# Performance work log

Measured on AMD Instinct MI355X. Metric: run time of the kernel, lower is better.

The kernel has to match this reference:

```python
import jax, jax.numpy as jnp
import numpy as np

IN_F = 512
OUT_F = 512

def setup_inputs() -> dict:
    key = jax.random.key(0)
    k1, k2, k3 = jax.random.split(key, 3)
    x = jax.random.normal(k1, (2, 512, IN_F), dtype=jnp.float32)
    # uniform init: a = sqrt(6 / (2 + out_features))
    a = float(np.sqrt(6.0 / (2.0 + OUT_F)))
    W = jax.random.uniform(k2, (OUT_F, IN_F), dtype=jnp.float32, minval=-a, maxval=a)
    bound = float(1.0 / np.sqrt(IN_F))
    b = jax.random.uniform(k3, (OUT_F,), dtype=jnp.float32, minval=-bound, maxval=bound)
    return {"x": x, "W": W, "b": b}

def reference(x, W, b):
    # MAM fully connected (beta == 0 path): for each (row, out-neuron),
    # C = max_k(x_k * w_ok) + min_k(x_k * w_ok), then add bias.
    xf = x.reshape(-1, x.shape[-1])            # (B, in)
    prod = xf[:, None, :] * W[None, :, :]      # (B, out, in) -- the large intermediate
    C = prod.max(axis=-1) + prod.min(axis=-1)  # (B, out)
    C = C + b[None, :]
    return C.reshape(x.shape[:-1] + (W.shape[0],))
```

## Files before the change

### kernel.cpp

```cpp
#include <hip/hip_runtime.h>
#include <math.h>


#define O_TOTAL 512
#define K_TOTAL 512
#define OBLK 64
#define NWAVE 4
#define RPW 2
#define RPB (NWAVE * RPW)
#define KCH 64
#define NCHUNK (K_TOTAL / KCH)

__device__ __forceinline__ void stage16(const float* g, float* lds, int lane) {
#if __has_builtin(__builtin_amdgcn_global_load_lds)
  (void)lane;
  __builtin_amdgcn_global_load_lds(
      (__attribute__((address_space(1))) unsigned int*)g,
      (__attribute__((address_space(3))) unsigned int*)lds, 16, 0, 0);
#else
  *reinterpret_cast<float4*>(lds + lane * 4) = *reinterpret_cast<const float4*>(g);
#endif
}

__global__ __launch_bounds__(256, 4)
void mam_fc_kernel(const float* __restrict__ x, const float* __restrict__ W,
                   const float* __restrict__ bias, float* __restrict__ out) {
  __shared__ float Wl[2][OBLK * KCH];
  __shared__ float Xl[2][RPB * KCH];

  const int t = threadIdx.x;
  const int lane = t & 63;
  const int wv = __builtin_amdgcn_readfirstlane(t >> 6);
  const int ob = blockIdx.x & 7;
  const int rg = blockIdx.x >> 3;
  const int o0 = ob * OBLK;
  const int rowBase = rg * RPB;

  const float* srcW[4];
  int dstWoff[4];
#pragma unroll
  for (int p = 0; p < 4; ++p) {
    const int orow = wv * 16 + p * 4 + (lane >> 4);
    const int g = (lane & 15) ^ (orow & 15);
    srcW[p] = W + (size_t)(o0 + orow) * K_TOTAL + g * 4;
    dstWoff[p] = (wv * 16 + p * 4) * KCH;
  }
  const float* srcX = x + (size_t)(rowBase + wv * 4 + (lane >> 4)) * K_TOTAL + (lane & 15) * 4;
  const int dstXoff = wv * 4 * KCH;

  float amax[RPW][2], amin[RPW][2];
#pragma unroll
  for (int r = 0; r < RPW; ++r) {
#pragma unroll
    for (int p = 0; p < 2; ++p) { amax[r][p] = -INFINITY; amin[r][p] = INFINITY; }
  }

  const unsigned baseW = (unsigned)(lane * (KCH * 4) + (lane & 15) * 16);
  const unsigned baseX = (unsigned)((wv * RPW) * (KCH * 4));

#pragma unroll
  for (int p = 0; p < 4; ++p) stage16(srcW[p], &Wl[0][dstWoff[p]], lane);
  if (wv < 2) stage16(srcX, &Xl[0][dstXoff], lane);
  __syncthreads();

#pragma unroll 1
  for (int c = 0; c < NCHUNK; ++c) {
    if (c + 1 < NCHUNK) {
      const int b = (c + 1) & 1;
      const int kOff = (c + 1) * KCH;
#pragma unroll
      for (int p = 0; p < 4; ++p) stage16(srcW[p] + kOff, &Wl[b][dstWoff[p]], lane);
      if (wv < 2) stage16(srcX + kOff, &Xl[b][dstXoff], lane);
    }

    const char* wb = (const char*)&Wl[c & 1][0];
    const char* xb = (const char*)&Xl[c & 1][0];
#pragma unroll
    for (int j = 0; j < KCH / 4; ++j) {
      const float4 w4 = *reinterpret_cast<const float4*>(wb + (baseW ^ (unsigned)(j * 16)));
#pragma unroll
      for (int r = 0; r < RPW; ++r) {
        const float4 x4 = *reinterpret_cast<const float4*>(xb + baseX + r * (KCH * 4) + j * 16);
        const float p0 = x4.x * w4.x;
        const float p1 = x4.y * w4.y;
        const float p2 = x4.z * w4.z;
        const float p3 = x4.w * w4.w;
        const int par = j & 1;
        amax[r][par] = fmaxf(fmaxf(fmaxf(fmaxf(amax[r][par], p0), p1), p2), p3);
        amin[r][par] = fminf(fminf(fminf(fminf(amin[r][par], p0), p1), p2), p3);
      }
    }
    __syncthreads();
  }

  const float bv = bias[o0 + lane];
#pragma unroll
  for (int r = 0; r < RPW; ++r) {
    const float mm = fmaxf(amax[r][0], amax[r][1]);
    const float nn = fminf(amin[r][0], amin[r][1]);
    out[(size_t)(rowBase + wv * RPW + r) * O_TOTAL + o0 + lane] = mm + nn + bv;
  }
}

extern "C" void kernel_launch(void* const* d_in, const int* in_sizes, int n_in,
                              void* d_out, int out_size, void* d_ws, size_t ws_size,
                              hipStream_t stream) {
  const float* x = (const float*)d_in[0];
  const float* W = (const float*)d_in[1];
  const float* b = (const float*)d_in[2];
  float* out = (float*)d_out;

  const int nrows = in_sizes[0] / K_TOTAL;
  const int nblocks = (O_TOTAL / OBLK) * (nrows / RPB);
  mam_fc_kernel<<<dim3(nblocks), dim3(256), 0, stream>>>(x, W, b, out);
}
```

Before: 22.08 us.

## Swap operand roles: lanes own rows, waves read uniform W rows directly

The kernel is restructured so each lane handles one input row (staged in LDS with an XOR swizzle) and each wave handles four output neurons whose weights are read straight from global memory at wave-uniform addresses, which can become scalar or broadcast loads. Tiles become 64 rows by 16 outputs, giving 512 blocks, and results go through an LDS transpose before a coalesced store with bias. The aim is to cut LDS traffic for W and raise per-lane reuse. The cost is global-load latency for W inside the inner loop, extra LDS for the output transpose, and occupancy hinted lower.

```diff
diff --git a/kernel.cpp b/kernel.cpp
--- a/kernel.cpp
+++ b/kernel.cpp
@@ -4,101 +4,100 @@
 
 #define O_TOTAL 512
 #define K_TOTAL 512
-#define OBLK 64
+#define ROWT 64
 #define NWAVE 4
-#define RPW 2
-#define RPB (NWAVE * RPW)
+#define OPW 4
+#define OUTT (NWAVE * OPW)
 #define KCH 64
 #define NCHUNK (K_TOTAL / KCH)
+#define NJ (KCH / 4)
 
-__device__ __forceinline__ void stage16(const float* g, float* lds, int lane) {
+__device__ __forceinline__ void stage16(const float* g, float* lds_base, int lane) {
 #if __has_builtin(__builtin_amdgcn_global_load_lds)
   (void)lane;
   __builtin_amdgcn_global_load_lds(
       (__attribute__((address_space(1))) unsigned int*)g,
-      (__attribute__((address_space(3))) unsigned int*)lds, 16, 0, 0);
+      (__attribute__((address_space(3))) unsigned int*)lds_base, 16, 0, 0);
 #else
-  *reinterpret_cast<float4*>(lds + lane * 4) = *reinterpret_cast<const float4*>(g);
+  *reinterpret_cast<float4*>(lds_base + lane * 4) = *reinterpret_cast<const float4*>(g);
 #endif
 }
 
-__global__ __launch_bounds__(256, 4)
+__global__ __launch_bounds__(256, 2)
 void mam_fc_kernel(const float* __restrict__ x, const float* __restrict__ W,
                    const float* __restrict__ bias, float* __restrict__ out) {
-  __shared__ float Wl[2][OBLK * KCH];
-  __shared__ float Xl[2][RPB * KCH];
+  __shared__ __align__(16) float Xl[2][ROWT * KCH];
+  __shared__ float Ot[ROWT][OUTT + 1];
 
   const int t = threadIdx.x;
   const int lane = t & 63;
   const int wv = __builtin_amdgcn_readfirstlane(t >> 6);
-  const int ob = blockIdx.x & 7;
-  const int rg = blockIdx.x >> 3;
-  const int o0 = ob * OBLK;
-  const int rowBase = rg * RPB;
+  const int ob = blockIdx.x & 31;
+  const int rg = blockIdx.x >> 5;
+  const int o0 = ob * OUTT;
+  const int row0 = rg * ROWT;
 
-  const float* srcW[4];
-  int dstWoff[4];
+  const float* srcX[4];
 #pragma unroll
   for (int p = 0; p < 4; ++p) {
-    const int orow = wv * 16 + p * 4 + (lane >> 4);
-    const int g = (lane & 15) ^ (orow & 15);
-    srcW[p] = W + (size_t)(o0 + orow) * K_TOTAL + g * 4;
-    dstWoff[p] = (wv * 16 + p * 4) * KCH;
-  }
-  const float* srcX = x + (size_t)(rowBase + wv * 4 + (lane >> 4)) * K_TOTAL + (lane & 15) * 4;
-  const int dstXoff = wv * 4 * KCH;
-
-  float amax[RPW][2], amin[RPW][2];
-#pragma unroll
-  for (int r = 0; r < RPW; ++r) {
-#pragma unroll
-    for (int p = 0; p < 2; ++p) { amax[r][p] = -INFINITY; amin[r][p] = INFINITY; }
+    const int r = wv * 16 + p * 4 + (lane >> 4);
+    const int g = (lane & 15) ^ (r & 15);
+    srcX[p] = x + (size_t)(row0 + r) * K_TOTAL + g * 4;
   }
 
-  const unsigned baseW = (unsigned)(lane * (KCH * 4) + (lane & 15) * 16);
-  const unsigned baseX = (unsigned)((wv * RPW) * (KCH * 4));
+  const float* Wo[OPW];
+#pragma unroll
+  for (int oi = 0; oi < OPW; ++oi)
+    Wo[oi] = W + (size_t)(o0 + wv * OPW + oi) * K_TOTAL;
+
+  float amax[OPW], amin[OPW];
+#pragma unroll
+  for (int oi = 0; oi < OPW; ++oi) { amax[oi] = -INFINITY; amin[oi] = INFINITY; }
+
+  const unsigned baseX = (unsigned)(lane * (KCH * 4) + (lane & 15) * 16);
 
 #pragma unroll
-  for (int p = 0; p < 4; ++p) stage16(srcW[p], &Wl[0][dstWoff[p]], lane);
-  if (wv < 2) stage16(srcX, &Xl[0][dstXoff], lane);
+  for (int p = 0; p < 4; ++p)
+    stage16(srcX[p], &Xl[0][wv * 1024 + p * 256], lane);
   __syncthreads();
 
 #pragma unroll 1
   for (int c = 0; c < NCHUNK; ++c) {
     if (c + 1 < NCHUNK) {
-      const int b = (c + 1) & 1;
       const int kOff = (c + 1) * KCH;
 #pragma unroll
-      for (int p = 0; p < 4; ++p) stage16(srcW[p] + kOff, &Wl[b][dstWoff[p]], lane);
-      if (wv < 2) stage16(srcX + kOff, &Xl[b][dstXoff], lane);
+      for (int p = 0; p < 4; ++p)
+        stage16(srcX[p] + kOff, &Xl[(c + 1) & 1][wv * 1024 + p * 256], lane);
     }
 
-    const char* wb = (const char*)&Wl[c & 1][0];
     const char* xb = (const char*)&Xl[c & 1][0];
 #pragma unroll
-    for (int j = 0; j < KCH / 4; ++j) {
-      const float4 w4 = *reinterpret_cast<const float4*>(wb + (baseW ^ (unsigned)(j * 16)));
+    for (int j = 0; j < NJ; ++j) {
+      const float4 x4 = *reinterpret_cast<const float4*>(xb + (baseX ^ (unsigned)(j * 16)));
 #pragma unroll
-      for (int r = 0; r < RPW; ++r) {
-        const float4 x4 = *reinterpret_cast<const float4*>(xb + baseX + r * (KCH * 4) + j * 16);
+      for (int oi = 0; oi < OPW; ++oi) {
+        const float4 w4 = *reinterpret_cast<const float4*>(Wo[oi] + c * KCH + j * 4);
         const float p0 = x4.x * w4.x;
         const float p1 = x4.y * w4.y;
         const float p2 = x4.z * w4.z;
         const float p3 = x4.w * w4.w;
-        const int par = j & 1;
-        amax[r][par] = fmaxf(fmaxf(fmaxf(fmaxf(amax[r][par], p0), p1), p2), p3);
-        amin[r][par] = fminf(fminf(fminf(fminf(amin[r][par], p0), p1), p2), p3);
+        amax[oi] = fmaxf(fmaxf(fmaxf(fmaxf(amax[oi], p0), p1), p2), p3);
+        amin[oi] = fminf(fminf(fminf(fminf(amin[oi], p0), p1), p2), p3);
       }
     }
     __syncthreads();
   }
 
-  const float bv = bias[o0 + lane];
 #pragma unroll
-  for (int r = 0; r < RPW; ++r) {
-    const float mm = fmaxf(amax[r][0], amax[r][1]);
-    const float nn = fminf(amin[r][0], amin[r][1]);
-    out[(size_t)(rowBase + wv * RPW + r) * O_TOTAL + o0 + lane] = mm + nn + bv;
+  for (int oi = 0; oi < OPW; ++oi)
+    Ot[lane][wv * OPW + oi] = amax[oi] + amin[oi];
+  __syncthreads();
+
+  const float bv = bias[o0 + (lane & 15)];
+#pragma unroll
+  for (int i = 0; i < 4; ++i) {
+    const int r = wv * 16 + i * 4 + (lane >> 4);
+    out[(size_t)(row0 + r) * O_TOTAL + o0 + (lane & 15)] = Ot[r][lane & 15] + bv;
   }
 }
 
@@ -111,6 +110,6 @@
   float* out = (float*)d_out;
 
   const int nrows = in_sizes[0] / K_TOTAL;
-  const int nblocks = (O_TOTAL / OBLK) * (nrows / RPB);
+  const int nblocks = (nrows / ROWT) * (O_TOTAL / OUTT);
   mam_fc_kernel<<<dim3(nblocks), dim3(256), 0, stream>>>(x, W, b, out);
 }
```

Measured after the change: 24.84 us. 1.12x slower.
